# Optimization experiments

Measured on AMD Instinct MI355X. Metric: run time of the kernel, lower is better.

Reference implementation:

```python
import jax, jax.numpy as jnp
import numpy as np
import math

BS, S, D = 1, 2048, 1024
H = 16
DK = D // H  # 64


def _log_sparse_neighbor_mask(seq_len):
    """mask[i,j]=True iff j==i, or j in [i-k, i) with k=seq_len//2, or i-j is a power of 2.
    Matches generate_log_sparse_plus_neighbors_mask(seq_len, seq_len//2)."""
    k = seq_len // 2
    i = jnp.arange(seq_len, dtype=jnp.int32)[:, None]
    j = jnp.arange(seq_len, dtype=jnp.int32)[None, :]
    diff = i - j
    neighbor = (diff >= 0) & (diff <= k)  # includes diagonal (diff==0)
    pow2 = (diff > 0) & ((diff & (diff - 1)) == 0)
    return neighbor | pow2  # [seq_len, seq_len] bool


def setup_inputs() -> dict:
    key = jax.random.key(0)
    ks = jax.random.split(key, 9)
    std = 0.02
    return {
        "Q": jax.random.normal(ks[0], (BS, S, D), dtype=jnp.float32),
        "Wq": jax.random.normal(ks[1], (D, H * DK), dtype=jnp.float32) * std,
        "bq": jnp.zeros((H * DK,), dtype=jnp.float32),
        "Wk": jax.random.normal(ks[2], (D, H * DK), dtype=jnp.float32) * std,
        "bk": jnp.zeros((H * DK,), dtype=jnp.float32),
        "Wv": jax.random.normal(ks[3], (D, H * DK), dtype=jnp.float32) * std,
        "bv": jnp.zeros((H * DK,), dtype=jnp.float32),
        "Wo": jax.random.normal(ks[4], (H * DK, D), dtype=jnp.float32) * std,
        "bo": jnp.zeros((D,), dtype=jnp.float32),
    }


def reference(Q, Wq, bq, Wk, bk, Wv, bv, Wo, bo):
    bs, s, d = Q.shape
    # QKV projections -> [bs, h, s, dk]
    q = (Q @ Wq + bq).reshape(bs, s, H, DK).transpose(0, 2, 1, 3)
    k = (Q @ Wk + bk).reshape(bs, s, H, DK).transpose(0, 2, 1, 3)
    v = (Q @ Wv + bv).reshape(bs, s, H, DK).transpose(0, 2, 1, 3)

    # log_sparse_attention: scale is 1/sqrt(d_k); mask regenerated internally
    mask = _log_sparse_neighbor_mask(s)  # [s, s] bool
    scores = jnp.einsum("bhqd,bhkd->bhqk", q, k) / math.sqrt(DK)
    scores = jnp.where(mask[None, None, :, :], scores, -jnp.inf)
    attn = jax.nn.softmax(scores, axis=-1)  # [bs, h, s, s]
    out = jnp.einsum("bhqk,bhkd->bhqd", attn, v)

    # merge heads + output projection
    out = out.transpose(0, 2, 1, 3).reshape(bs, s, H * DK)
    out = out @ Wo + bo
    return (out, attn)
```

## Files before the change

kernel.cpp:

```cpp
#include <hip/hip_runtime.h>

#define SEQ 2048
#define DM 1024
#define NH 16
#define DKH 64
#define BAND 1024
#define QKV 3072
#define PBW 1064

typedef __attribute__((ext_vector_type(8))) __bf16 bf16x8;
typedef __attribute__((ext_vector_type(4))) __bf16 bf16x4;
typedef __attribute__((ext_vector_type(4))) float f32x4;

static __device__ __forceinline__ f32x4 mfma16(bf16x8 a, bf16x8 b, f32x4 c) {
  return __builtin_amdgcn_mfma_f32_16x16x32_bf16(a, b, c, 0, 0, 0);
}

#define GLOAD16(gp, lp)                                                        \
  __builtin_amdgcn_global_load_lds(                                            \
      (const __attribute__((address_space(1))) void*)(gp),                     \
      (__attribute__((address_space(3))) void*)(lp), 16, 0, 0)

struct PrepArgs {
  const float* win[4];
  __bf16* wout[4];
  const float* Q;
  __bf16* Qb;
};
__global__ void prep(PrepArgs P) {
  int z = blockIdx.z;
  if (z < 4) {
    __shared__ float t[32][33];
    const float* in = P.win[z];
    __bf16* out = P.wout[z];
    int c0 = blockIdx.x * 32, r0 = blockIdx.y * 32;
    int tx = threadIdx.x, ty = threadIdx.y;
    for (int r = ty; r < 32; r += 8)
      t[r][tx] = in[(size_t)(r0 + r) * DM + c0 + tx];
    __syncthreads();
    for (int r = ty; r < 32; r += 8)
      out[(size_t)(c0 + r) * DM + r0 + tx] = (__bf16)t[tx][r];
  } else {
    int t = threadIdx.y * 32 + threadIdx.x;
    int base = (blockIdx.y * 32 + blockIdx.x) * 512 + t;
#pragma unroll
    for (int u = 0; u < 2; u++) {
      int i = base + u * 256;
      float4 v = reinterpret_cast<const float4*>(P.Q)[i];
      bf16x4 o = {(__bf16)v.x, (__bf16)v.y, (__bf16)v.z, (__bf16)v.w};
      reinterpret_cast<bf16x4*>(P.Qb)[i] = o;
    }
  }
}

template <int BM, int BN, bool BF16OUT, bool VOUT>
__global__ __launch_bounds__(256) void gemm_lds(
    const __bf16* __restrict__ A, const __bf16* __restrict__ BT,
    const float* __restrict__ b0, const float* __restrict__ b1,
    const float* __restrict__ b2, float* __restrict__ Cf,
    __bf16* __restrict__ Cb, __bf16* __restrict__ VT, int M, int N, int K) {
  constexpr int BK = 64;
  constexpr int FM = BM / 32;
  constexpr int FN = BN / 32;
  constexpr int LA = BM * BK * 2 / (256 * 16);
  constexpr int LB = BN * BK * 2 / (256 * 16);
  __shared__ __bf16 lA[2][BM * BK];
  __shared__ __bf16 lB[2][BN * BK];
  int tid = threadIdx.x;
  int lane = tid & 63;
  int l15 = lane & 15, lg = lane >> 4;
  int w = tid >> 6;
  int nwg = gridDim.x * gridDim.y;
  int bid = blockIdx.y * gridDim.x + blockIdx.x;
  int swz = (bid & 7) * (nwg >> 3) + (bid >> 3);
  int bx = swz % gridDim.x;
  int by = swz / gridDim.x;
  int row0 = by * BM;
  int col0 = bx * BN;
  int sec = col0 >> 10;
  const float* bias = sec == 0 ? b0 : (sec == 1 ? b1 : b2);
  int cbase = col0 & (DM - 1);
  int wr = (w >> 1) * (BM / 2);
  int wc = (w & 1) * (BN / 2);
  f32x4 acc[FM][FN] = {};

  auto stage = [&](int b, int kt) {
#pragma unroll
    for (int s = 0; s < LA; s++) {
      int u = tid + s * 256;
      int r = u >> 3;
      int cc = (u & 7) ^ (r & 7);
      GLOAD16(A + (size_t)(row0 + r) * K + kt * BK + cc * 8,
              (char*)lA[b] + u * 16);
    }
#pragma unroll
    for (int s = 0; s < LB; s++) {
      int u = tid + s * 256;
      int r = u >> 3;
      int cc = (u & 7) ^ (r & 7);
      GLOAD16(BT + (size_t)(col0 + r) * K + kt * BK + cc * 8,
              (char*)lB[b] + u * 16);
    }
  };

  const int T = K / BK;
  stage(0, 0);
  stage(1, 1);
  for (int t = 0; t < T; t++) {
    if (t + 1 < T)
      asm volatile("s_waitcnt vmcnt(%0)" ::"i"(LA + LB) : "memory");
    else
      asm volatile("s_waitcnt vmcnt(0)" ::: "memory");
    __builtin_amdgcn_s_barrier();
    int cur = t & 1;
    bf16x8 af[2][FM], bfr[2][FN];
#pragma unroll
    for (int kh = 0; kh < 2; kh++) {
#pragma unroll
      for (int mi = 0; mi < FM; mi++) {
        int r = wr + mi * 16 + l15;
        af[kh][mi] = *(const bf16x8*)((const char*)lA[cur] + r * 128 +
                                      ((((kh << 2) | lg) ^ (r & 7)) << 4));
      }
#pragma unroll
      for (int ni = 0; ni < FN; ni++) {
        int r = wc + ni * 16 + l15;
        bfr[kh][ni] = *(const bf16x8*)((const char*)lB[cur] + r * 128 +
                                       ((((kh << 2) | lg) ^ (r & 7)) << 4));
      }
    }
#pragma unroll
    for (int kh = 0; kh < 2; kh++)
#pragma unroll
      for (int mi = 0; mi < FM; mi++)
#pragma unroll
        for (int ni = 0; ni < FN; ni++)
          acc[mi][ni] = mfma16(af[kh][mi], bfr[kh][ni], acc[mi][ni]);
    __builtin_amdgcn_s_barrier();
    if (t + 2 < T) stage(cur, t + 2);
  }

  if (VOUT && sec == 2) {
#pragma unroll
    for (int mi = 0; mi < FM; mi++) {
      int row = row0 + wr + mi * 16 + lg * 4;
#pragma unroll
      for (int ni = 0; ni < FN; ni++) {
        int hd = cbase + wc + ni * 16 + l15;
        float b = bias[hd];
        bf16x4 pk;
#pragma unroll
        for (int r = 0; r < 4; r++) pk[r] = (__bf16)(acc[mi][ni][r] + b);
        *(bf16x4*)&VT[(size_t)hd * SEQ + row] = pk;
      }
    }
    return;
  }
#pragma unroll
  for (int mi = 0; mi < FM; mi++) {
    int row = row0 + wr + mi * 16 + lg * 4;
#pragma unroll
    for (int ni = 0; ni < FN; ni++) {
      int col = col0 + wc + ni * 16 + l15;
      float b = bias[(cbase + wc + ni * 16 + l15) & (DM - 1)];
#pragma unroll
      for (int r = 0; r < 4; r++) {
        float v = acc[mi][ni][r] + b;
        if constexpr (BF16OUT)
          Cb[(size_t)(row + r) * N + col] = (__bf16)v;
        else
          Cf[(size_t)(row + r) * N + col] = v;
      }
    }
  }
}

__global__ __launch_bounds__(256) void attn_fused(
    const __bf16* __restrict__ qkvb, const __bf16* __restrict__ VT,
    float* __restrict__ attn_out, __bf16* __restrict__ pvb) {
  __shared__ __bf16 pbuf[16][PBW];
  __shared__ float wsum[4][16];
  __shared__ float sinv[16];

  int nwg = gridDim.x * gridDim.y;
  int bid = blockIdx.y * gridDim.x + blockIdx.x;
  int swz = (bid & 7) * (nwg >> 3) + (bid >> 3);
  int h = swz / (SEQ / 16);
  int i0 = (swz % (SEQ / 16)) * 16;

  int tid = threadIdx.x, lane = tid & 63, w = tid >> 6;
  int l15 = lane & 15, lg = lane >> 4;

  int jlo = i0 - BAND;
  if (jlo < 0) jlo = 0;
  int ntiles = (i0 + 16 - jlo) >> 4;
  int ktiles = (ntiles + 1) & ~1;
  int n = ntiles * 16;

  const __bf16* qptr = qkvb + (size_t)(i0 + l15) * QKV + h * DKH + lg * 8;
  bf16x8 aq0 = *(const bf16x8*)qptr;
  bf16x8 aq1 = *(const bf16x8*)(qptr + 32);
  const __bf16* kbase = qkvb + DM + h * DKH + lg * 8;

  float sm[4] = {0.f, 0.f, 0.f, 0.f};
  for (int t = w; t < ntiles; t += 4) {
    int jb = jlo + t * 16;
    const __bf16* kptr = kbase + (size_t)(jb + l15) * QKV;
    f32x4 acc = {0.f, 0.f, 0.f, 0.f};
    acc = mfma16(aq0, *(const bf16x8*)kptr, acc);
    acc = mfma16(aq1, *(const bf16x8*)(kptr + 32), acc);
    int col = jb + l15;
    int x = jb - jlo + l15;
#pragma unroll
    for (int r = 0; r < 4; r++) {
      int i = i0 + lg * 4 + r;
      float e = 0.f;
      if (col <= i && i - col <= BAND) {
        e = __expf(acc[r] * 0.125f);
        sm[r] += e;
      }
      pbuf[lg * 4 + r][x] = (__bf16)e;
    }
  }
  if (ktiles != ntiles) pbuf[tid >> 4][n + (tid & 15)] = (__bf16)0.f;
#pragma unroll
  for (int o = 1; o < 16; o <<= 1)
#pragma unroll
    for (int r = 0; r < 4; r++) sm[r] += __shfl_xor(sm[r], o);
  if (l15 == 0)
#pragma unroll
    for (int r = 0; r < 4; r++) wsum[w][lg * 4 + r] = sm[r];
  __syncthreads();
  if (tid < 16)
    sinv[tid] = 1.f / (wsum[0][tid] + wsum[1][tid] + wsum[2][tid] + wsum[3][tid]);
  __syncthreads();

  f32x4* abase = (f32x4*)(attn_out + ((size_t)h * SEQ + i0) * SEQ);
  for (int idx = tid; idx < 16 * (SEQ / 4); idx += 256) {
    int row = idx >> 9;
    int j4 = idx & 511;
    int x = j4 * 4 - jlo;
    bool valid = (unsigned)x < (unsigned)n;
    int xc = valid ? x : 0;
    bf16x4 v4 = *(const bf16x4*)&pbuf[row][xc];
    float inv = valid ? sinv[row] : 0.f;
    f32x4 o = {(float)v4[0] * inv, (float)v4[1] * inv, (float)v4[2] * inv,
               (float)v4[3] * inv};
    __builtin_nontemporal_store(o, abase + idx);
  }

  f32x4 acc = {0.f, 0.f, 0.f, 0.f};
  int d0 = w * 16;
  const __bf16* vtp = VT + ((size_t)h * DKH + d0 + l15) * SEQ;
  for (int kt = 0; kt < ktiles; kt += 2) {
    int kk = kt * 16;
    bf16x8 pa = *(const bf16x8*)&pbuf[l15][kk + lg * 8];
    int jj = jlo + kk + lg * 8;
    bf16x8 vf = {};
    if (jj < SEQ) vf = *(const bf16x8*)(vtp + jj);
    acc = mfma16(pa, vf, acc);
  }
#pragma unroll
  for (int r = 0; r < 4; r++) {
    int row = lg * 4 + r;
    float inv = sinv[row];
    pvb[(size_t)(i0 + row) * DM + h * DKH + d0 + l15] = (__bf16)(acc[r] * inv);
  }
}

extern "C" void kernel_launch(void* const* d_in, const int* in_sizes, int n_in,
                              void* d_out, int out_size, void* d_ws,
                              size_t ws_size, hipStream_t stream) {
  const float* Q = (const float*)d_in[0];
  const float* Wq = (const float*)d_in[1];
  const float* bq = (const float*)d_in[2];
  const float* Wk = (const float*)d_in[3];
  const float* bk = (const float*)d_in[4];
  const float* Wv = (const float*)d_in[5];
  const float* bv = (const float*)d_in[6];
  const float* Wo = (const float*)d_in[7];
  const float* bo = (const float*)d_in[8];
  float* out_proj = (float*)d_out;
  float* attn_out = out_proj + (size_t)SEQ * DM;

  char* ws = (char*)d_ws;
  size_t off = 0;
  auto alloc = [&](size_t bytes) {
    void* p = ws + off;
    off = (off + bytes + 255) & ~(size_t)255;
    return p;
  };
  __bf16* Qb    = (__bf16*)alloc((size_t)SEQ * DM * 2);
  __bf16* WqkvT = (__bf16*)alloc((size_t)QKV * DM * 2);
  __bf16* WoT   = (__bf16*)alloc((size_t)DM * DM * 2);
  __bf16* qkvb  = (__bf16*)alloc((size_t)SEQ * QKV * 2);
  __bf16* VT    = (__bf16*)alloc((size_t)NH * DKH * SEQ * 2);
  __bf16* pvb   = (__bf16*)alloc((size_t)SEQ * DM * 2);

  PrepArgs P;
  P.win[0] = Wq; P.win[1] = Wk; P.win[2] = Wv; P.win[3] = Wo;
  P.wout[0] = WqkvT;
  P.wout[1] = WqkvT + (size_t)DM * DM;
  P.wout[2] = WqkvT + (size_t)2 * DM * DM;
  P.wout[3] = WoT;
  P.Q = Q;
  P.Qb = Qb;
  prep<<<dim3(32, 32, 5), dim3(32, 8), 0, stream>>>(P);

  gemm_lds<64, 128, true, true><<<dim3(QKV / 128, SEQ / 64), 256, 0, stream>>>(
      Qb, WqkvT, bq, bk, bv, nullptr, qkvb, VT, SEQ, QKV, DM);

  attn_fused<<<dim3(SEQ / 16, NH), 256, 0, stream>>>(qkvb, VT, attn_out, pvb);

  gemm_lds<64, 64, false, false><<<dim3(DM / 64, SEQ / 64), 256, 0, stream>>>(
      pvb, WoT, bo, bo, bo, out_proj, nullptr, nullptr, SEQ, DM, DM);
}
```

Measured before the change: 120.5 us.

## Overlap masked-zero attention writes with GEMM main loops

The attention kernel now writes only the band columns of each attention row. The zero regions of the attention matrix are written as nontemporal stores interleaved into the K-loops of the QKV and output-projection GEMMs, with adjusted vmcnt waits. Heads are split across the two GEMMs, and out-of-range slots go to a dump buffer. The aim is to hide the large zero-fill write traffic behind GEMM compute. The cost is extra memory traffic competing with the GEMM loads and more fragile indexing and waitcnt logic.

Result: slower. 130.6 us (+8.4%).

```diff
diff --git a/kernel.cpp b/kernel.cpp
--- a/kernel.cpp
+++ b/kernel.cpp
@@ -53,12 +53,13 @@
   }
 }
 
-template <int BM, int BN, bool BF16OUT, bool VOUT>
+template <int BM, int BN, bool BF16OUT, bool VOUT, int ZPI, int NPAIR, int HOFF>
 __global__ __launch_bounds__(256) void gemm_lds(
     const __bf16* __restrict__ A, const __bf16* __restrict__ BT,
     const float* __restrict__ b0, const float* __restrict__ b1,
     const float* __restrict__ b2, float* __restrict__ Cf,
-    __bf16* __restrict__ Cb, __bf16* __restrict__ VT, int M, int N, int K) {
+    __bf16* __restrict__ Cb, __bf16* __restrict__ VT,
+    f32x4* __restrict__ attnz, f32x4* __restrict__ dumpz, int M, int N, int K) {
   constexpr int BK = 64;
   constexpr int FM = BM / 32;
   constexpr int FN = BN / 32;
@@ -82,6 +83,12 @@
   int cbase = col0 & (DM - 1);
   int wr = (w >> 1) * (BM / 2);
   int wc = (w & 1) * (BN / 2);
+  int zb = swz & 127;
+  int hb = swz >> 7;
+  int zL = 4 * zb - 256;
+  if (zL < 0) zL = 0;
+  int zR = 4 * zb + 4;
+  f32x4* dmp = dumpz + (swz & 255);
   f32x4 acc[FM][FN] = {};
 
   auto stage = [&](int b, int kt) {
@@ -107,10 +114,15 @@
   stage(0, 0);
   stage(1, 1);
   for (int t = 0; t < T; t++) {
-    if (t + 1 < T)
+    if (t == T - 1) {
+      asm volatile("s_waitcnt vmcnt(%0)" ::"i"(2 * ZPI) : "memory");
+    } else if (t <= 2 || ZPI == 0) {
       asm volatile("s_waitcnt vmcnt(%0)" ::"i"(LA + LB) : "memory");
-    else
-      asm volatile("s_waitcnt vmcnt(0)" ::: "memory");
+    } else if (t == 3) {
+      asm volatile("s_waitcnt vmcnt(%0)" ::"i"(LA + LB + ZPI) : "memory");
+    } else {
+      asm volatile("s_waitcnt vmcnt(%0)" ::"i"(LA + LB + 2 * ZPI) : "memory");
+    }
     __builtin_amdgcn_s_barrier();
     int cur = t & 1;
     bf16x8 af[2][FM], bfr[2][FN];
@@ -138,6 +150,28 @@
           acc[mi][ni] = mfma16(af[kh][mi], bfr[kh][ni], acc[mi][ni]);
     __builtin_amdgcn_s_barrier();
     if (t + 2 < T) stage(cur, t + 2);
+    if constexpr (ZPI > 0) {
+      if (t >= 2) {
+        f32x4 zz = {0.f, 0.f, 0.f, 0.f};
+        int ibase = (t - 2) * (ZPI * 256) + tid;
+#pragma unroll
+        for (int z = 0; z < ZPI; z++) {
+          int idx = ibase + z * 256;
+          int pair = idx >> 13;
+          int row = (idx >> 9) & 15;
+          int c = idx & 511;
+          int j4 = c < zL ? c : zR + (c - zL);
+          bool ok = (idx < NPAIR * 8192) && (j4 < 512);
+          if (ok) {
+            int hh = HOFF + hb + pair * 6;
+            __builtin_nontemporal_store(
+                zz, attnz + ((size_t)hh * SEQ + zb * 16 + row) * 512 + j4);
+          } else {
+            *dmp = zz;
+          }
+        }
+      }
+    }
   }
 
   if (VOUT && sec == 2) {
@@ -235,18 +269,18 @@
     sinv[tid] = 1.f / (wsum[0][tid] + wsum[1][tid] + wsum[2][tid] + wsum[3][tid]);
   __syncthreads();
 
-  f32x4* abase = (f32x4*)(attn_out + ((size_t)h * SEQ + i0) * SEQ);
-  for (int idx = tid; idx < 16 * (SEQ / 4); idx += 256) {
-    int row = idx >> 9;
-    int j4 = idx & 511;
-    int x = j4 * 4 - jlo;
-    bool valid = (unsigned)x < (unsigned)n;
-    int xc = valid ? x : 0;
-    bf16x4 v4 = *(const bf16x4*)&pbuf[row][xc];
-    float inv = valid ? sinv[row] : 0.f;
-    f32x4 o = {(float)v4[0] * inv, (float)v4[1] * inv, (float)v4[2] * inv,
-               (float)v4[3] * inv};
-    __builtin_nontemporal_store(o, abase + idx);
+  float* arow = attn_out + ((size_t)h * SEQ + i0) * SEQ;
+  int jl4 = jlo >> 2;
+  int jh4 = (i0 + 16) >> 2;
+  for (int row = 0; row < 16; row++) {
+    f32x4* a4 = (f32x4*)(arow + (size_t)row * SEQ);
+    float inv = sinv[row];
+    for (int j4 = jl4 + tid; j4 < jh4; j4 += 256) {
+      bf16x4 v4 = *(const bf16x4*)&pbuf[row][j4 * 4 - jlo];
+      f32x4 o = {(float)v4[0] * inv, (float)v4[1] * inv, (float)v4[2] * inv,
+                 (float)v4[3] * inv};
+      __builtin_nontemporal_store(o, a4 + j4);
+    }
   }
 
   f32x4 acc = {0.f, 0.f, 0.f, 0.f};
@@ -296,6 +330,7 @@
   __bf16* qkvb  = (__bf16*)alloc((size_t)SEQ * QKV * 2);
   __bf16* VT    = (__bf16*)alloc((size_t)NH * DKH * SEQ * 2);
   __bf16* pvb   = (__bf16*)alloc((size_t)SEQ * DM * 2);
+  f32x4*  dumpz = (f32x4*)alloc(4096 * 16);
 
   PrepArgs P;
   P.win[0] = Wq; P.win[1] = Wk; P.win[2] = Wv; P.win[3] = Wo;
@@ -307,11 +342,15 @@
   P.Qb = Qb;
   prep<<<dim3(32, 32, 5), dim3(32, 8), 0, stream>>>(P);
 
-  gemm_lds<64, 128, true, true><<<dim3(QKV / 128, SEQ / 64), 256, 0, stream>>>(
-      Qb, WqkvT, bq, bk, bv, nullptr, qkvb, VT, SEQ, QKV, DM);
+  gemm_lds<64, 128, true, true, 5, 2, 0>
+      <<<dim3(QKV / 128, SEQ / 64), 256, 0, stream>>>(
+          Qb, WqkvT, bq, bk, bv, nullptr, qkvb, VT, (f32x4*)attn_out, dumpz,
+          SEQ, QKV, DM);
 
   attn_fused<<<dim3(SEQ / 16, NH), 256, 0, stream>>>(qkvb, VT, attn_out, pvb);
 
-  gemm_lds<64, 64, false, false><<<dim3(DM / 64, SEQ / 64), 256, 0, stream>>>(
-      pvb, WoT, bo, bo, bo, out_proj, nullptr, nullptr, SEQ, DM, DM);
-}
+  gemm_lds<64, 64, false, false, 3, 1, 12>
+      <<<dim3(DM / 64, SEQ / 64), 256, 0, stream>>>(
+          pvb, WoT, bo, bo, bo, out_proj, nullptr, nullptr, (f32x4*)attn_out,
+          dumpz, SEQ, DM, DM);
+}
```
